# Kernel optimization log

Hardware: AMD Instinct MI355X
Metric: run time of the kernel (lower is better)

The kernel has to match this reference:

```python
import jax, jax.numpy as jnp
import numpy as np

N_SECTIONS = 4  # cascaded biquads (direct-form II transposed), 2 states each


def setup_inputs() -> dict:
    key = jax.random.key(0)
    k1, k2, k3 = jax.random.split(key, 3)
    B, T = 512, 32768
    x = jax.random.normal(k1, (B, T, 1), dtype=jnp.float32)
    # scale coefficients so the IIR recurrence stays stable over T steps
    b = jax.random.normal(k2, (N_SECTIONS, 3), dtype=jnp.float32) * 0.5
    a = jax.random.normal(k3, (N_SECTIONS, 2), dtype=jnp.float32) * 0.1
    return {"x": x, "b": b, "a": a}


def reference(x, b, a):
    # x: (B, T, 1) -> per-step scalar signal per batch element.
    # Cascade of N_SECTIONS biquads, direct-form II transposed:
    #   y  = b0*u + s1
    #   s1' = b1*u - a1*y + s2
    #   s2' = b2*u - a2*y
    B = x.shape[0]
    xs = x[..., 0].T  # (T, B): scan over time, vectorized over batch
    init_states = jnp.zeros((N_SECTIONS, 2, B), dtype=x.dtype)

    def step(states, u_t):
        sig = u_t  # (B,)
        new_states = []
        for k in range(N_SECTIONS):  # fixed small structural loop
            s1, s2 = states[k, 0], states[k, 1]
            y = b[k, 0] * sig + s1
            ns1 = b[k, 1] * sig - a[k, 0] * y + s2
            ns2 = b[k, 2] * sig - a[k, 1] * y
            new_states.append(jnp.stack([ns1, ns2]))
            sig = y
        return jnp.stack(new_states), sig

    _, ys = jax.lax.scan(step, init_states, xs)  # ys: (T, B)
    return ys.T[..., None]  # (B, T, 1), matching out_sequence.unsqueeze(-1)
```

## Files before the change

kernel.cpp:

```cpp
#include <hip/hip_runtime.h>


namespace {
constexpr int NS     = 4;
constexpr int BATCH  = 512;
constexpr int TLEN   = 32768;
constexpr int NSTATE = 8;
constexpr int P      = 512;
constexpr int L      = TLEN / P;
constexpr int LQ     = L / 4;
constexpr int LOG2P  = 9;
constexpr int LOG2L  = 6;
}

__device__ __forceinline__ void load_coefs(const float* __restrict__ bc,
                                           const float* __restrict__ ac,
                                           float b0[NS], float b1[NS], float b2[NS],
                                           float a1[NS], float a2[NS]) {
#pragma unroll
  for (int k = 0; k < NS; ++k) {
    b0[k] = bc[3 * k];
    b1[k] = bc[3 * k + 1];
    b2[k] = bc[3 * k + 2];
    a1[k] = ac[2 * k];
    a2[k] = ac[2 * k + 1];
  }
}

__device__ __forceinline__ float step_cascade(float sig,
                                              const float b0[NS], const float b1[NS],
                                              const float b2[NS], const float a1[NS],
                                              const float a2[NS],
                                              float s1[NS], float s2[NS]) {
#pragma unroll
  for (int k = 0; k < NS; ++k) {
    float y = fmaf(b0[k], sig, s1[k]);
    s1[k]   = fmaf(-a1[k], y, fmaf(b1[k], sig, s2[k]));
    s2[k]   = fmaf(-a2[k], y, b2[k] * sig);
    sig = y;
  }
  return sig;
}

#define CO b0, b1, b2, a1, a2

__device__ __forceinline__ void adv4(const float4 u,
                                     const float b0[NS], const float b1[NS],
                                     const float b2[NS], const float a1[NS],
                                     const float a2[NS], float s1[NS], float s2[NS]) {
  (void)step_cascade(u.x, CO, s1, s2);
  (void)step_cascade(u.y, CO, s1, s2);
  (void)step_cascade(u.z, CO, s1, s2);
  (void)step_cascade(u.w, CO, s1, s2);
}

__device__ __forceinline__ float4 out4(const float4 u,
                                       const float b0[NS], const float b1[NS],
                                       const float b2[NS], const float a1[NS],
                                       const float a2[NS], float s1[NS], float s2[NS]) {
  float4 y;
  y.x = step_cascade(u.x, CO, s1, s2);
  y.y = step_cascade(u.y, CO, s1, s2);
  y.z = step_cascade(u.z, CO, s1, s2);
  y.w = step_cascade(u.w, CO, s1, s2);
  return y;
}

__global__ __launch_bounds__(P) void k_fused(const float* __restrict__ x,
                                             const float* __restrict__ bc,
                                             const float* __restrict__ ac,
                                             float* __restrict__ out) {
  __shared__ float4 arena[4096];
  float* Msf = reinterpret_cast<float*>(arena);
  float* Wf  = reinterpret_cast<float*>(arena) + 576;

  const int t = threadIdx.x;
  float b0[NS], b1[NS], b2[NS], a1[NS], a2[NS];
  load_coefs(bc, ac, b0, b1, b2, a1, a2);

  if (t < 64) {
    const int r = t >> 3, c = t & 7;
    float p1[NS] = {0.f, 0.f, 0.f, 0.f};
    float p2[NS] = {0.f, 0.f, 0.f, 0.f};
    if (c & 1) p2[c >> 1] = 1.0f; else p1[c >> 1] = 1.0f;
    (void)step_cascade(0.0f, CO, p1, p2);
    float m = (r & 1) ? p2[r >> 1] : p1[r >> 1];
    for (int it = 0; it < LOG2L + LOG2P - 1; ++it) {
      float acc = 0.0f;
#pragma unroll
      for (int k = 0; k < NSTATE; ++k)
        acc = fmaf(__shfl(m, r * 8 + k), __shfl(m, k * 8 + c), acc);
      m = acc;
      if (it >= LOG2L - 1) Msf[(it - (LOG2L - 1)) * 64 + t] = m;
    }
  }

  const float4* __restrict__ gp =
      reinterpret_cast<const float4*>(x) + ((size_t)blockIdx.x * P + t) * LQ;
  float s1[NS] = {0.f, 0.f, 0.f, 0.f};
  float s2[NS] = {0.f, 0.f, 0.f, 0.f};
  float4 ld[4];
#pragma unroll
  for (int j = 0; j < 4; ++j) ld[j] = gp[j];
#pragma unroll
  for (int q0 = 0; q0 < LQ; q0 += 4) {
#pragma unroll
    for (int j = 0; j < 4; ++j) {
      const float4 u = ld[j];
      if (q0 + 4 + j < LQ) ld[j] = gp[q0 + 4 + j];
      adv4(u, CO, s1, s2);
    }
  }

  float w[NSTATE];
#pragma unroll
  for (int k = 0; k < NS; ++k) { w[2 * k] = s1[k]; w[2 * k + 1] = s2[k]; }

  for (int d = 0; d < LOG2P; ++d) {
#pragma unroll
    for (int r = 0; r < NSTATE; ++r) Wf[t * 9 + r] = w[r];
    __syncthreads();
    if (t >= (1 << d)) {
      const int src = (t - (1 << d)) * 9;
      float prev[NSTATE];
#pragma unroll
      for (int r = 0; r < NSTATE; ++r) prev[r] = Wf[src + r];
#pragma unroll
      for (int r = 0; r < NSTATE; ++r) {
        float acc = w[r];
#pragma unroll
        for (int k = 0; k < NSTATE; ++k)
          acc = fmaf(Msf[d * 64 + r * 8 + k], prev[k], acc);
        w[r] = acc;
      }
    }
    __syncthreads();
  }

#pragma unroll
  for (int r = 0; r < NSTATE; ++r) Wf[t * 9 + r] = w[r];
  __syncthreads();
  {
    const int src = (t == 0 ? 0 : t - 1) * 9;
#pragma unroll
    for (int k = 0; k < NS; ++k) {
      s1[k] = (t == 0) ? 0.0f : Wf[src + 2 * k];
      s2[k] = (t == 0) ? 0.0f : Wf[src + 2 * k + 1];
    }
  }
  __syncthreads();

  const int lane = t & 63;
  const int wv   = t >> 6;
  float4* __restrict__ Lb = arena + (wv << 9);
  float4* __restrict__ gout = reinterpret_cast<float4*>(out) +
      ((size_t)blockIdx.x * P + (wv << 6)) * LQ;

#pragma unroll
  for (int j = 0; j < 4; ++j) ld[j] = gp[j];

#pragma unroll
  for (int q = 0; q < 8; ++q) {
    const float4 u = ld[q & 3];
    ld[q & 3] = gp[q + 4];
    Lb[lane * 8 + (q ^ (lane & 7))] = out4(u, CO, s1, s2);
  }
  asm volatile("s_waitcnt lgkmcnt(0)" ::: "memory");
  __builtin_amdgcn_sched_barrier(0);
#pragma unroll
  for (int k = 0; k < 8; ++k) {
    const int s = k * 64 + lane;
    const int c = s >> 3, q = s & 7;
    gout[c * 16 + q] = Lb[c * 8 + (q ^ (c & 7))];
  }
  asm volatile("s_waitcnt lgkmcnt(0)" ::: "memory");
  __builtin_amdgcn_sched_barrier(0);

#pragma unroll
  for (int q = 8; q < 16; ++q) {
    const float4 u = ld[q & 3];
    if (q + 4 < 16) ld[q & 3] = gp[q + 4];
    Lb[lane * 8 + ((q & 7) ^ (lane & 7))] = out4(u, CO, s1, s2);
  }
  asm volatile("s_waitcnt lgkmcnt(0)" ::: "memory");
  __builtin_amdgcn_sched_barrier(0);
#pragma unroll
  for (int k = 0; k < 8; ++k) {
    const int s = k * 64 + lane;
    const int c = s >> 3, q = s & 7;
    gout[c * 16 + 8 + q] = Lb[c * 8 + (q ^ (c & 7))];
  }
}

extern "C" void kernel_launch(void* const* d_in, const int* in_sizes, int n_in,
                              void* d_out, int out_size, void* d_ws, size_t ws_size,
                              hipStream_t stream) {
  const float* x  = (const float*)d_in[0];
  const float* bc = (const float*)d_in[1];
  const float* ac = (const float*)d_in[2];
  float* out = (float*)d_out;

  k_fused<<<BATCH, P, 0, stream>>>(x, bc, ac, out);
}
```

Baseline: 42.22 us.

## Stage input loads through swizzled LDS for coalescing and double-buffer the scan

Both the reduction pass and the output pass now load input with coalesced float4 reads, where consecutive lanes read consecutive addresses. The data is transposed through a swizzled per-wave LDS tile, replacing the old per-thread strided chunk reads. The matrix-power precompute now runs redundantly in every wave after the first pass instead of serially in wave 0 up front. The Hillis-Steele scan ping-pongs between two LDS buffers, dropping one barrier per level. In exchange it adds extra LDS traffic and waitcnt fences, and the per-wave matrix squaring costs some compute.

```diff
diff --git a/kernel.cpp b/kernel.cpp
--- a/kernel.cpp
+++ b/kernel.cpp
@@ -13,6 +13,9 @@
 constexpr int LOG2L  = 6;
 }
 
+#define LGKM0 do { asm volatile("s_waitcnt lgkmcnt(0)" ::: "memory"); \
+                   __builtin_amdgcn_sched_barrier(0); } while (0)
+
 __device__ __forceinline__ void load_coefs(const float* __restrict__ bc,
                                            const float* __restrict__ ac,
                                            float b0[NS], float b1[NS], float b2[NS],
@@ -72,59 +75,82 @@
                                              float* __restrict__ out) {
   __shared__ float4 arena[4096];
   float* Msf = reinterpret_cast<float*>(arena);
-  float* Wf  = reinterpret_cast<float*>(arena) + 576;
-
-  const int t = threadIdx.x;
+  float* W0f = reinterpret_cast<float*>(arena) + 576;
+  float* W1f = reinterpret_cast<float*>(arena) + 5184;
+
+  const int t    = threadIdx.x;
+  const int lane = t & 63;
+  const int wv   = t >> 6;
+  float4* __restrict__ Lb = arena + (wv << 9);
+
   float b0[NS], b1[NS], b2[NS], a1[NS], a2[NS];
   load_coefs(bc, ac, b0, b1, b2, a1, a2);
 
-  if (t < 64) {
-    const int r = t >> 3, c = t & 7;
+  const int m   = lane & 7;
+  const int g0  = (wv * 64 + (lane >> 3)) * LQ + m;
+  const int ls0 = (lane >> 3) * 8 + (m ^ ((lane >> 3) & 7));
+  const int rs0 = lane * 8;
+
+  const float4* __restrict__ gx =
+      reinterpret_cast<const float4*>(x) + (size_t)blockIdx.x * (P * LQ);
+  float4* __restrict__ gy =
+      reinterpret_cast<float4*>(out) + (size_t)blockIdx.x * (P * LQ);
+
+  float4 tmp[8];
+#pragma unroll
+  for (int j = 0; j < 8; ++j) tmp[j] = gx[g0 + 128 * j];
+  float s1[NS] = {0.f, 0.f, 0.f, 0.f};
+  float s2[NS] = {0.f, 0.f, 0.f, 0.f};
+#pragma unroll
+  for (int j = 0; j < 8; ++j) Lb[ls0 + 64 * j] = tmp[j];
+#pragma unroll
+  for (int j = 0; j < 8; ++j) tmp[j] = gx[g0 + 8 + 128 * j];
+  LGKM0;
+#pragma unroll
+  for (int q = 0; q < 8; ++q) adv4(Lb[rs0 + (q ^ (lane & 7))], CO, s1, s2);
+  LGKM0;
+#pragma unroll
+  for (int j = 0; j < 8; ++j) Lb[ls0 + 64 * j] = tmp[j];
+  LGKM0;
+#pragma unroll
+  for (int q = 0; q < 8; ++q) adv4(Lb[rs0 + (q ^ (lane & 7))], CO, s1, s2);
+
+  float w[NSTATE];
+#pragma unroll
+  for (int k = 0; k < NS; ++k) { w[2 * k] = s1[k]; w[2 * k + 1] = s2[k]; }
+
+  __syncthreads();
+
+  {
+    const int r = lane >> 3, cc = lane & 7;
     float p1[NS] = {0.f, 0.f, 0.f, 0.f};
     float p2[NS] = {0.f, 0.f, 0.f, 0.f};
-    if (c & 1) p2[c >> 1] = 1.0f; else p1[c >> 1] = 1.0f;
+    if (cc & 1) p2[cc >> 1] = 1.0f; else p1[cc >> 1] = 1.0f;
     (void)step_cascade(0.0f, CO, p1, p2);
-    float m = (r & 1) ? p2[r >> 1] : p1[r >> 1];
+    float mm = (r & 1) ? p2[r >> 1] : p1[r >> 1];
     for (int it = 0; it < LOG2L + LOG2P - 1; ++it) {
       float acc = 0.0f;
 #pragma unroll
       for (int k = 0; k < NSTATE; ++k)
-        acc = fmaf(__shfl(m, r * 8 + k), __shfl(m, k * 8 + c), acc);
-      m = acc;
-      if (it >= LOG2L - 1) Msf[(it - (LOG2L - 1)) * 64 + t] = m;
+        acc = fmaf(__shfl(mm, r * 8 + k), __shfl(mm, k * 8 + cc), acc);
+      mm = acc;
+      asm volatile("" :: "v"(mm));
+      if (t < 64 && it >= LOG2L - 1) Msf[(it - (LOG2L - 1)) * 64 + t] = mm;
     }
   }
 
-  const float4* __restrict__ gp =
-      reinterpret_cast<const float4*>(x) + ((size_t)blockIdx.x * P + t) * LQ;
-  float s1[NS] = {0.f, 0.f, 0.f, 0.f};
-  float s2[NS] = {0.f, 0.f, 0.f, 0.f};
-  float4 ld[4];
-#pragma unroll
-  for (int j = 0; j < 4; ++j) ld[j] = gp[j];
-#pragma unroll
-  for (int q0 = 0; q0 < LQ; q0 += 4) {
-#pragma unroll
-    for (int j = 0; j < 4; ++j) {
-      const float4 u = ld[j];
-      if (q0 + 4 + j < LQ) ld[j] = gp[q0 + 4 + j];
-      adv4(u, CO, s1, s2);
-    }
-  }
-
-  float w[NSTATE];
-#pragma unroll
-  for (int k = 0; k < NS; ++k) { w[2 * k] = s1[k]; w[2 * k + 1] = s2[k]; }
-
+#pragma unroll
+  for (int r = 0; r < NSTATE; ++r) W0f[t * 9 + r] = w[r];
+  __syncthreads();
+#pragma unroll
   for (int d = 0; d < LOG2P; ++d) {
-#pragma unroll
-    for (int r = 0; r < NSTATE; ++r) Wf[t * 9 + r] = w[r];
-    __syncthreads();
+    const float* Ws = (d & 1) ? W1f : W0f;
+    float* Wd       = (d & 1) ? W0f : W1f;
     if (t >= (1 << d)) {
       const int src = (t - (1 << d)) * 9;
       float prev[NSTATE];
 #pragma unroll
-      for (int r = 0; r < NSTATE; ++r) prev[r] = Wf[src + r];
+      for (int r = 0; r < NSTATE; ++r) prev[r] = Ws[src + r];
 #pragma unroll
       for (int r = 0; r < NSTATE; ++r) {
         float acc = w[r];
@@ -134,62 +160,49 @@
         w[r] = acc;
       }
     }
+#pragma unroll
+    for (int r = 0; r < NSTATE; ++r) Wd[t * 9 + r] = w[r];
     __syncthreads();
   }
 
-#pragma unroll
-  for (int r = 0; r < NSTATE; ++r) Wf[t * 9 + r] = w[r];
-  __syncthreads();
   {
     const int src = (t == 0 ? 0 : t - 1) * 9;
 #pragma unroll
     for (int k = 0; k < NS; ++k) {
-      s1[k] = (t == 0) ? 0.0f : Wf[src + 2 * k];
-      s2[k] = (t == 0) ? 0.0f : Wf[src + 2 * k + 1];
+      s1[k] = (t == 0) ? 0.0f : W1f[src + 2 * k];
+      s2[k] = (t == 0) ? 0.0f : W1f[src + 2 * k + 1];
     }
   }
+
+#pragma unroll
+  for (int j = 0; j < 8; ++j) tmp[j] = gx[g0 + 128 * j];
   __syncthreads();
 
-  const int lane = t & 63;
-  const int wv   = t >> 6;
-  float4* __restrict__ Lb = arena + (wv << 9);
-  float4* __restrict__ gout = reinterpret_cast<float4*>(out) +
-      ((size_t)blockIdx.x * P + (wv << 6)) * LQ;
-
-#pragma unroll
-  for (int j = 0; j < 4; ++j) ld[j] = gp[j];
-
+#pragma unroll
+  for (int j = 0; j < 8; ++j) Lb[ls0 + 64 * j] = tmp[j];
+#pragma unroll
+  for (int j = 0; j < 8; ++j) tmp[j] = gx[g0 + 8 + 128 * j];
+  LGKM0;
 #pragma unroll
   for (int q = 0; q < 8; ++q) {
-    const float4 u = ld[q & 3];
-    ld[q & 3] = gp[q + 4];
-    Lb[lane * 8 + (q ^ (lane & 7))] = out4(u, CO, s1, s2);
-  }
-  asm volatile("s_waitcnt lgkmcnt(0)" ::: "memory");
-  __builtin_amdgcn_sched_barrier(0);
-#pragma unroll
-  for (int k = 0; k < 8; ++k) {
-    const int s = k * 64 + lane;
-    const int c = s >> 3, q = s & 7;
-    gout[c * 16 + q] = Lb[c * 8 + (q ^ (c & 7))];
-  }
-  asm volatile("s_waitcnt lgkmcnt(0)" ::: "memory");
-  __builtin_amdgcn_sched_barrier(0);
-
-#pragma unroll
-  for (int q = 8; q < 16; ++q) {
-    const float4 u = ld[q & 3];
-    if (q + 4 < 16) ld[q & 3] = gp[q + 4];
-    Lb[lane * 8 + ((q & 7) ^ (lane & 7))] = out4(u, CO, s1, s2);
-  }
-  asm volatile("s_waitcnt lgkmcnt(0)" ::: "memory");
-  __builtin_amdgcn_sched_barrier(0);
-#pragma unroll
-  for (int k = 0; k < 8; ++k) {
-    const int s = k * 64 + lane;
-    const int c = s >> 3, q = s & 7;
-    gout[c * 16 + 8 + q] = Lb[c * 8 + (q ^ (c & 7))];
-  }
+    const int s = rs0 + (q ^ (lane & 7));
+    Lb[s] = out4(Lb[s], CO, s1, s2);
+  }
+  LGKM0;
+#pragma unroll
+  for (int j = 0; j < 8; ++j) gy[g0 + 128 * j] = Lb[ls0 + 64 * j];
+  LGKM0;
+#pragma unroll
+  for (int j = 0; j < 8; ++j) Lb[ls0 + 64 * j] = tmp[j];
+  LGKM0;
+#pragma unroll
+  for (int q = 0; q < 8; ++q) {
+    const int s = rs0 + (q ^ (lane & 7));
+    Lb[s] = out4(Lb[s], CO, s1, s2);
+  }
+  LGKM0;
+#pragma unroll
+  for (int j = 0; j < 8; ++j) gy[g0 + 8 + 128 * j] = Lb[ls0 + 64 * j];
 }
 
 extern "C" void kernel_launch(void* const* d_in, const int* in_sizes, int n_in,
```

Measured after the change: 87.74 us. 2.08x slower.

## Stage whole input tile in LDS once to avoid re-reading x from global

Applied to the files above, without the earlier changes.

Adds a new kernel that loads each block's entire input chunk (128 KB) into dynamic LDS, using global_load_lds when the builtin is available. Both scan passes then read from LDS, and the outputs are written back in place and stored coalesced, so x is no longer read from global memory twice. In exchange it needs about 160 KB of LDS per block, which allows only one block per CU, and there is a fallback to the old kernel if the attribute set or launch fails. It also puts a host hipFuncSetAttribute call on every launch.

```diff
diff --git a/kernel.cpp b/kernel.cpp
--- a/kernel.cpp
+++ b/kernel.cpp
@@ -11,7 +11,18 @@
 constexpr int LQ     = L / 4;
 constexpr int LOG2P  = 9;
 constexpr int LOG2L  = 6;
-}
+constexpr int XF4    = P * LQ;
+constexpr size_t DYN_LDS = (size_t)XF4 * 16 + (576 + 4608) * 4;
+}
+
+#if defined(__has_builtin)
+#  if __has_builtin(__builtin_amdgcn_global_load_lds)
+#    define USE_GLL 1
+#  endif
+#endif
+#ifndef USE_GLL
+#  define USE_GLL 0
+#endif
 
 __device__ __forceinline__ void load_coefs(const float* __restrict__ bc,
                                            const float* __restrict__ ac,
@@ -66,17 +77,56 @@
   return y;
 }
 
-__global__ __launch_bounds__(P) void k_fused(const float* __restrict__ x,
-                                             const float* __restrict__ bc,
-                                             const float* __restrict__ ac,
-                                             float* __restrict__ out) {
-  __shared__ float4 arena[4096];
-  float* Msf = reinterpret_cast<float*>(arena);
-  float* Wf  = reinterpret_cast<float*>(arena) + 576;
-
-  const int t = threadIdx.x;
+__global__ __launch_bounds__(P, 2) void k_fused_res(const float* __restrict__ x,
+                                                    const float* __restrict__ bc,
+                                                    const float* __restrict__ ac,
+                                                    float* __restrict__ out) {
+  extern __shared__ float4 arena[];
+  float* Msf = reinterpret_cast<float*>(arena + XF4);
+  float* Wf  = Msf + 576;
+
+  const int t    = threadIdx.x;
+  const int lane = t & 63;
+  const int wv   = t >> 6;
+  float4* __restrict__ Lb = arena + (wv << 10);
+
   float b0[NS], b1[NS], b2[NS], a1[NS], a2[NS];
   load_coefs(bc, ac, b0, b1, b2, a1, a2);
+
+  const float4* __restrict__ gx = reinterpret_cast<const float4*>(x) +
+      (size_t)blockIdx.x * XF4 + ((size_t)wv << 10);
+  float4* __restrict__ gy = reinterpret_cast<float4*>(out) +
+      (size_t)blockIdx.x * XF4 + ((size_t)wv << 10);
+
+#if USE_GLL
+#pragma unroll
+  for (int j = 0; j < 16; ++j) {
+    const int s  = j * 64 + lane;
+    const int cc = s >> 4;
+    const int q  = (s & 15) ^ (cc & 15);
+    const float4* g = gx + cc * 16 + q;
+    __builtin_amdgcn_global_load_lds(
+        (const __attribute__((address_space(1))) void*)g,
+        (__attribute__((address_space(3))) void*)&Lb[j * 64], 16, 0, 0);
+  }
+  asm volatile("s_waitcnt vmcnt(0)" ::: "memory");
+  __builtin_amdgcn_sched_barrier(0);
+#else
+  {
+    float4 tmp[16];
+#pragma unroll
+    for (int j = 0; j < 16; ++j) {
+      const int s  = j * 64 + lane;
+      const int cc = s >> 4;
+      const int q  = (s & 15) ^ (cc & 15);
+      tmp[j] = gx[cc * 16 + q];
+    }
+#pragma unroll
+    for (int j = 0; j < 16; ++j) Lb[j * 64 + lane] = tmp[j];
+    asm volatile("s_waitcnt lgkmcnt(0)" ::: "memory");
+    __builtin_amdgcn_sched_barrier(0);
+  }
+#endif
 
   if (t < 64) {
     const int r = t >> 3, c = t & 7;
@@ -95,6 +145,100 @@
     }
   }
 
+  float s1[NS] = {0.f, 0.f, 0.f, 0.f};
+  float s2[NS] = {0.f, 0.f, 0.f, 0.f};
+#pragma unroll
+  for (int q = 0; q < LQ; ++q)
+    adv4(Lb[lane * 16 + (q ^ (lane & 15))], CO, s1, s2);
+
+  float w[NSTATE];
+#pragma unroll
+  for (int k = 0; k < NS; ++k) { w[2 * k] = s1[k]; w[2 * k + 1] = s2[k]; }
+
+  for (int d = 0; d < LOG2P; ++d) {
+#pragma unroll
+    for (int r = 0; r < NSTATE; ++r) Wf[t * 9 + r] = w[r];
+    __syncthreads();
+    if (t >= (1 << d)) {
+      const int src = (t - (1 << d)) * 9;
+      float prev[NSTATE];
+#pragma unroll
+      for (int r = 0; r < NSTATE; ++r) prev[r] = Wf[src + r];
+#pragma unroll
+      for (int r = 0; r < NSTATE; ++r) {
+        float acc = w[r];
+#pragma unroll
+        for (int k = 0; k < NSTATE; ++k)
+          acc = fmaf(Msf[d * 64 + r * 8 + k], prev[k], acc);
+        w[r] = acc;
+      }
+    }
+    __syncthreads();
+  }
+
+#pragma unroll
+  for (int r = 0; r < NSTATE; ++r) Wf[t * 9 + r] = w[r];
+  __syncthreads();
+  {
+    const int src = (t == 0 ? 0 : t - 1) * 9;
+#pragma unroll
+    for (int k = 0; k < NS; ++k) {
+      s1[k] = (t == 0) ? 0.0f : Wf[src + 2 * k];
+      s2[k] = (t == 0) ? 0.0f : Wf[src + 2 * k + 1];
+    }
+  }
+
+#pragma unroll
+  for (int q = 0; q < LQ; ++q) {
+    const int s = lane * 16 + (q ^ (lane & 15));
+    Lb[s] = out4(Lb[s], CO, s1, s2);
+  }
+  asm volatile("s_waitcnt lgkmcnt(0)" ::: "memory");
+  __builtin_amdgcn_sched_barrier(0);
+
+#pragma unroll
+  for (int h = 0; h < 2; ++h) {
+    float4 tq[8];
+#pragma unroll
+    for (int j = 0; j < 8; ++j) {
+      const int g  = (h * 8 + j) * 64 + lane;
+      const int cc = g >> 4;
+      tq[j] = Lb[cc * 16 + ((g & 15) ^ (cc & 15))];
+    }
+#pragma unroll
+    for (int j = 0; j < 8; ++j) gy[(h * 8 + j) * 64 + lane] = tq[j];
+  }
+}
+
+__global__ __launch_bounds__(P) void k_fused(const float* __restrict__ x,
+                                             const float* __restrict__ bc,
+                                             const float* __restrict__ ac,
+                                             float* __restrict__ out) {
+  __shared__ float4 arena[4096];
+  float* Msf = reinterpret_cast<float*>(arena);
+  float* Wf  = reinterpret_cast<float*>(arena) + 576;
+
+  const int t = threadIdx.x;
+  float b0[NS], b1[NS], b2[NS], a1[NS], a2[NS];
+  load_coefs(bc, ac, b0, b1, b2, a1, a2);
+
+  if (t < 64) {
+    const int r = t >> 3, c = t & 7;
+    float p1[NS] = {0.f, 0.f, 0.f, 0.f};
+    float p2[NS] = {0.f, 0.f, 0.f, 0.f};
+    if (c & 1) p2[c >> 1] = 1.0f; else p1[c >> 1] = 1.0f;
+    (void)step_cascade(0.0f, CO, p1, p2);
+    float m = (r & 1) ? p2[r >> 1] : p1[r >> 1];
+    for (int it = 0; it < LOG2L + LOG2P - 1; ++it) {
+      float acc = 0.0f;
+#pragma unroll
+      for (int k = 0; k < NSTATE; ++k)
+        acc = fmaf(__shfl(m, r * 8 + k), __shfl(m, k * 8 + c), acc);
+      m = acc;
+      if (it >= LOG2L - 1) Msf[(it - (LOG2L - 1)) * 64 + t] = m;
+    }
+  }
+
   const float4* __restrict__ gp =
       reinterpret_cast<const float4*>(x) + ((size_t)blockIdx.x * P + t) * LQ;
   float s1[NS] = {0.f, 0.f, 0.f, 0.f};
@@ -200,5 +344,16 @@
   const float* ac = (const float*)d_in[2];
   float* out = (float*)d_out;
 
-  k_fused<<<BATCH, P, 0, stream>>>(x, bc, ac, out);
-}
+  hipError_t arc = hipFuncSetAttribute(
+      reinterpret_cast<const void*>(k_fused_res),
+      hipFuncAttributeMaxDynamicSharedMemorySize, (int)DYN_LDS);
+
+  bool ok = (arc == hipSuccess);
+  if (ok) {
+    k_fused_res<<<BATCH, P, DYN_LDS, stream>>>(x, bc, ac, out);
+    if (hipGetLastError() != hipSuccess) ok = false;
+  }
+  if (!ok) {
+    k_fused<<<BATCH, P, 0, stream>>>(x, bc, ac, out);
+  }
+}
```

Measured after the change: 51.06 us. 20.9% more time.

## Stage input through LDS with coalesced global_load_lds instead of strided per-thread loads

Applied to the files above, without the earlier changes.

Each thread used to read its own contiguous chunk of the input straight from global memory. Those per-thread float4 loads are strided by the chunk length, so accesses across lanes are poorly coalesced. Now each wave loads its half-tiles into LDS with coalesced, swizzled loads, using global_load_lds when the builtin exists, and threads read their chunk back from LDS in both the scan pass and the output pass. The matrix powers are kept in registers and written to LDS only after a barrier, because the arena is now reused for staging. This adds LDS traffic and vmcnt waits that serialize the loads with compute, and there is no cross-half double buffering.

```diff
diff --git a/kernel.cpp b/kernel.cpp
--- a/kernel.cpp
+++ b/kernel.cpp
@@ -11,7 +11,22 @@
 constexpr int LQ     = L / 4;
 constexpr int LOG2P  = 9;
 constexpr int LOG2L  = 6;
-}
+constexpr int NSQ    = LOG2L + LOG2P - 1;
+}
+
+#if defined(__has_builtin)
+#  if __has_builtin(__builtin_amdgcn_global_load_lds)
+#    define USE_GLL 1
+#  endif
+#endif
+#ifndef USE_GLL
+#  define USE_GLL 0
+#endif
+
+#define WAIT_VM0 do { asm volatile("s_waitcnt vmcnt(0)" ::: "memory"); \
+                      __builtin_amdgcn_sched_barrier(0); } while (0)
+#define WAIT_LGKM0 do { asm volatile("s_waitcnt lgkmcnt(0)" ::: "memory"); \
+                        __builtin_amdgcn_sched_barrier(0); } while (0)
 
 __device__ __forceinline__ void load_coefs(const float* __restrict__ bc,
                                            const float* __restrict__ ac,
@@ -66,6 +81,28 @@
   return y;
 }
 
+__device__ __forceinline__ void stage_ht(const float4* __restrict__ gx_w,
+                                         float4* R, int lane, int ht) {
+#if USE_GLL
+#pragma unroll
+  for (int j = 0; j < 8; ++j) {
+    const int cc = j * 8 + (lane >> 3);
+    const int qq = lane & 7;
+    const float4* g = gx_w + cc * 16 + ht * 8 + (qq ^ (cc & 7));
+    __builtin_amdgcn_global_load_lds(
+        (const __attribute__((address_space(1))) void*)g,
+        (__attribute__((address_space(3))) void*)&R[j * 64], 16, 0, 0);
+  }
+#else
+#pragma unroll
+  for (int j = 0; j < 8; ++j) {
+    const int cc = j * 8 + (lane >> 3);
+    const int qq = lane & 7;
+    R[j * 64 + lane] = gx_w[cc * 16 + ht * 8 + (qq ^ (cc & 7))];
+  }
+#endif
+}
+
 __global__ __launch_bounds__(P) void k_fused(const float* __restrict__ x,
                                              const float* __restrict__ bc,
                                              const float* __restrict__ ac,
@@ -74,47 +111,63 @@
   float* Msf = reinterpret_cast<float*>(arena);
   float* Wf  = reinterpret_cast<float*>(arena) + 576;
 
-  const int t = threadIdx.x;
+  const int t    = threadIdx.x;
+  const int lane = t & 63;
+  const int wv   = t >> 6;
+  const int swz  = lane & 7;
+  float4* __restrict__ R = arena + (wv << 9);
+
   float b0[NS], b1[NS], b2[NS], a1[NS], a2[NS];
   load_coefs(bc, ac, b0, b1, b2, a1, a2);
 
+  const float4* __restrict__ gx_w = reinterpret_cast<const float4*>(x) +
+      (size_t)blockIdx.x * (P * LQ) + ((size_t)wv << 10);
+  float4* __restrict__ gy_w = reinterpret_cast<float4*>(out) +
+      (size_t)blockIdx.x * (P * LQ) + ((size_t)wv << 10);
+
+  stage_ht(gx_w, R, lane, 0);
+
+  float mpow[9];
+#pragma unroll
+  for (int i = 0; i < 9; ++i) mpow[i] = 0.0f;
   if (t < 64) {
-    const int r = t >> 3, c = t & 7;
+    const int r = lane >> 3, c = lane & 7;
     float p1[NS] = {0.f, 0.f, 0.f, 0.f};
     float p2[NS] = {0.f, 0.f, 0.f, 0.f};
     if (c & 1) p2[c >> 1] = 1.0f; else p1[c >> 1] = 1.0f;
     (void)step_cascade(0.0f, CO, p1, p2);
     float m = (r & 1) ? p2[r >> 1] : p1[r >> 1];
-    for (int it = 0; it < LOG2L + LOG2P - 1; ++it) {
+#pragma unroll
+    for (int it = 0; it < NSQ; ++it) {
       float acc = 0.0f;
 #pragma unroll
       for (int k = 0; k < NSTATE; ++k)
         acc = fmaf(__shfl(m, r * 8 + k), __shfl(m, k * 8 + c), acc);
       m = acc;
-      if (it >= LOG2L - 1) Msf[(it - (LOG2L - 1)) * 64 + t] = m;
-    }
-  }
-
-  const float4* __restrict__ gp =
-      reinterpret_cast<const float4*>(x) + ((size_t)blockIdx.x * P + t) * LQ;
+      if (it >= LOG2L - 1) mpow[it - (LOG2L - 1)] = m;
+    }
+  }
+
   float s1[NS] = {0.f, 0.f, 0.f, 0.f};
   float s2[NS] = {0.f, 0.f, 0.f, 0.f};
-  float4 ld[4];
-#pragma unroll
-  for (int j = 0; j < 4; ++j) ld[j] = gp[j];
-#pragma unroll
-  for (int q0 = 0; q0 < LQ; q0 += 4) {
-#pragma unroll
-    for (int j = 0; j < 4; ++j) {
-      const float4 u = ld[j];
-      if (q0 + 4 + j < LQ) ld[j] = gp[q0 + 4 + j];
-      adv4(u, CO, s1, s2);
-    }
-  }
+  WAIT_VM0;
+#pragma unroll
+  for (int q = 0; q < 8; ++q) adv4(R[lane * 8 + (q ^ swz)], CO, s1, s2);
+  WAIT_LGKM0;
+  stage_ht(gx_w, R, lane, 1);
+  WAIT_VM0;
+#pragma unroll
+  for (int q = 0; q < 8; ++q) adv4(R[lane * 8 + (q ^ swz)], CO, s1, s2);
 
   float w[NSTATE];
 #pragma unroll
   for (int k = 0; k < NS; ++k) { w[2 * k] = s1[k]; w[2 * k + 1] = s2[k]; }
+
+  __syncthreads();
+  if (t < 64) {
+#pragma unroll
+    for (int d = 0; d < LOG2P; ++d) Msf[d * 64 + t] = mpow[d];
+  }
 
   for (int d = 0; d < LOG2P; ++d) {
 #pragma unroll
@@ -150,45 +203,24 @@
   }
   __syncthreads();
 
-  const int lane = t & 63;
-  const int wv   = t >> 6;
-  float4* __restrict__ Lb = arena + (wv << 9);
-  float4* __restrict__ gout = reinterpret_cast<float4*>(out) +
-      ((size_t)blockIdx.x * P + (wv << 6)) * LQ;
-
-#pragma unroll
-  for (int j = 0; j < 4; ++j) ld[j] = gp[j];
-
-#pragma unroll
-  for (int q = 0; q < 8; ++q) {
-    const float4 u = ld[q & 3];
-    ld[q & 3] = gp[q + 4];
-    Lb[lane * 8 + (q ^ (lane & 7))] = out4(u, CO, s1, s2);
-  }
-  asm volatile("s_waitcnt lgkmcnt(0)" ::: "memory");
-  __builtin_amdgcn_sched_barrier(0);
-#pragma unroll
-  for (int k = 0; k < 8; ++k) {
-    const int s = k * 64 + lane;
-    const int c = s >> 3, q = s & 7;
-    gout[c * 16 + q] = Lb[c * 8 + (q ^ (c & 7))];
-  }
-  asm volatile("s_waitcnt lgkmcnt(0)" ::: "memory");
-  __builtin_amdgcn_sched_barrier(0);
-
-#pragma unroll
-  for (int q = 8; q < 16; ++q) {
-    const float4 u = ld[q & 3];
-    if (q + 4 < 16) ld[q & 3] = gp[q + 4];
-    Lb[lane * 8 + ((q & 7) ^ (lane & 7))] = out4(u, CO, s1, s2);
-  }
-  asm volatile("s_waitcnt lgkmcnt(0)" ::: "memory");
-  __builtin_amdgcn_sched_barrier(0);
-#pragma unroll
-  for (int k = 0; k < 8; ++k) {
-    const int s = k * 64 + lane;
-    const int c = s >> 3, q = s & 7;
-    gout[c * 16 + 8 + q] = Lb[c * 8 + (q ^ (c & 7))];
+#pragma unroll
+  for (int ht = 0; ht < 2; ++ht) {
+    stage_ht(gx_w, R, lane, ht);
+    WAIT_VM0;
+#pragma unroll
+    for (int q = 0; q < 8; ++q) {
+      const int s = lane * 8 + (q ^ swz);
+      R[s] = out4(R[s], CO, s1, s2);
+    }
+    WAIT_LGKM0;
+#pragma unroll
+    for (int j = 0; j < 8; ++j) {
+      const int cc = j * 8 + (lane >> 3);
+      const int qq = lane & 7;
+      const float4 v = R[j * 64 + lane];
+      gy_w[cc * 16 + ht * 8 + (qq ^ (cc & 7))] = v;
+    }
+    if (ht == 0) WAIT_LGKM0;
   }
 }
 
```

Result: no change. 41.48 us (-1.8%).
